# Kernel optimization log

Measured on AMD Instinct MI355X. Metric: run time of the kernel, lower is better.

Reference implementation:

```python
import jax, jax.numpy as jnp
import numpy as np


def setup_inputs() -> dict:
    key = jax.random.key(0)
    ks = jax.random.split(key, 6)
    B, N_IN, N_OUT, C_IN, C_OUT, S, NNZ = 16, 6250, 25000, 64, 64, 9, 75000
    x = jax.random.normal(ks[0], (B, N_IN, C_IN), dtype=jnp.float32)
    trans_values = jax.random.uniform(ks[1], (NNZ,), dtype=jnp.float32)
    trans_row = jax.random.randint(ks[2], (NNZ,), 0, N_OUT, dtype=jnp.int32)
    trans_col = jax.random.randint(ks[3], (NNZ,), 0, N_IN, dtype=jnp.int32)
    spiral_indices = jax.random.randint(ks[4], (N_OUT, S), 0, N_OUT, dtype=jnp.int32)
    # Linear(S*C_IN -> C_OUT), kaiming-ish scale
    W = jax.random.normal(ks[5], (S * C_IN, C_OUT), dtype=jnp.float32) * (1.0 / np.sqrt(S * C_IN))
    b = jnp.zeros((C_OUT,), dtype=jnp.float32)
    return {"x": x, "trans_values": trans_values, "trans_row": trans_row,
            "trans_col": trans_col, "spiral_indices": spiral_indices,
            "W": W, "b": b, "n_out": N_OUT}


def reference(x, trans_values, trans_row, trans_col, spiral_indices, W, b, n_out):
    B, N_in, C = x.shape
    # Pool: gather cols, scale by sparse values, scatter-add to rows
    gathered = x[:, trans_col, :] * trans_values[None, :, None]        # [B, nnz, C]
    pooled = jnp.zeros((B, n_out, C), x.dtype).at[:, trans_row].add(gathered)  # [B, n_out, C]
    # SpiralConv: gather spiral neighborhoods, flatten, linear
    S = spiral_indices.shape[1]
    feat = pooled[:, spiral_indices, :].reshape(B, n_out, S * C)       # [B, n_out, S*C]
    out = feat @ W + b                                                 # [B, n_out, C_out]
    return jax.nn.elu(out)
```

## Files before the change

### kernel.cpp

```cpp
#include <hip/hip_runtime.h>

#define B_     16
#define N_IN_  6250
#define N_OUT_ 25000
#define C_     64
#define S_     9
#define NNZ_   75000
#define MT_    391
#define BROW_  584

typedef __bf16 bf16x8 __attribute__((ext_vector_type(8)));
typedef float floatx4 __attribute__((ext_vector_type(4)));

__device__ inline void async_copy16(const void* g, void* l) {
    __builtin_amdgcn_global_load_lds(
        (const __attribute__((address_space(1))) void*)g,
        (__attribute__((address_space(3))) void*)l, 16, 0, 0);
}


__global__ void hist_kernel(const int* __restrict__ rows, int* __restrict__ counts, int nnz) {
    int i = blockIdx.x * blockDim.x + threadIdx.x;
    if (i < nnz) atomicAdd(&counts[rows[i]], 1);
}

__global__ void scan1_kernel(const int* __restrict__ counts, int* __restrict__ offsets,
                             int* __restrict__ bsum, int n) {
    __shared__ int wsum[16];
    int t = threadIdx.x;
    int wid = t >> 6, lane = t & 63;
    int i = blockIdx.x * 1024 + t;
    int v = (i < n) ? counts[i] : 0;
    int s = v;
    #pragma unroll
    for (int d = 1; d < 64; d <<= 1) {
        int u = __shfl_up(s, d, 64);
        if (lane >= d) s += u;
    }
    if (lane == 63) wsum[wid] = s;
    __syncthreads();
    if (wid == 0 && lane < 16) {
        int ws = wsum[lane];
        #pragma unroll
        for (int d = 1; d < 16; d <<= 1) {
            int u = __shfl_up(ws, d, 64);
            if (lane >= d) ws += u;
        }
        wsum[lane] = ws;
    }
    __syncthreads();
    int wave_off = (wid == 0) ? 0 : wsum[wid - 1];
    int incl = s + wave_off;
    if (i < n) offsets[i] = incl - v;
    if (t == 1023) bsum[blockIdx.x] = incl;
}

__global__ void scan2_kernel(int* __restrict__ bsum, int* __restrict__ offsets, int nblk, int n) {
    if (threadIdx.x == 0) {
        int t = 0;
        for (int i = 0; i < nblk; ++i) { int v = bsum[i]; bsum[i] = t; t += v; }
        offsets[n] = t;
    }
}

__global__ void scan3_kernel(int* __restrict__ offsets, const int* __restrict__ bsum,
                             int* __restrict__ cursor, int n) {
    int i = blockIdx.x * 1024 + threadIdx.x;
    if (i < n) {
        int o = offsets[i] + bsum[blockIdx.x];
        offsets[i] = o;
        cursor[i] = o;
    }
}

__global__ void fill_kernel(const int* __restrict__ rows, const int* __restrict__ cols,
                            const float* __restrict__ vals, int* __restrict__ cursor,
                            int* __restrict__ ecol, float* __restrict__ eval, int nnz) {
    int i = blockIdx.x * blockDim.x + threadIdx.x;
    if (i < nnz) {
        int p = atomicAdd(&cursor[rows[i]], 1);
        ecol[p] = cols[i];
        eval[p] = vals[i];
    }
}

__global__ __launch_bounds__(256) void pool_kernel(
        const float* __restrict__ x, const int* __restrict__ offsets,
        const int* __restrict__ ecol, const float* __restrict__ eval,
        __bf16* __restrict__ pooled) {
    __shared__ int   scol[64];
    __shared__ float sval[64];
    int row = blockIdx.x;
    int t = threadIdx.x;
    int c = t & 63, bq = t >> 6;
    int beg = offsets[row], end = offsets[row + 1];
    int count = end - beg;

    float acc[4] = {0.f, 0.f, 0.f, 0.f};
    for (int base = 0; base < count; base += 64) {
        int nb = min(64, count - base);
        if (t < nb) {
            scol[t] = ecol[beg + base + t];
            sval[t] = eval[beg + base + t];
        }
        __syncthreads();
        for (int k = 0; k < nb; ++k) {
            int col = scol[k];
            float v = sval[k];
            const float* xp = x + ((size_t)col * C_ + c);
            #pragma unroll
            for (int j = 0; j < 4; ++j) {
                acc[j] += xp[(size_t)(bq * 4 + j) * N_IN_ * C_] * v;
            }
        }
        __syncthreads();
    }
    #pragma unroll
    for (int j = 0; j < 4; ++j) {
        pooled[((size_t)(bq * 4 + j) * N_OUT_ + row) * C_ + c] = (__bf16)acc[j];
    }
}

__global__ void convw_kernel(const float* __restrict__ W, __bf16* __restrict__ Wt) {
    int i = blockIdx.x * blockDim.x + threadIdx.x;
    if (i < 576 * 64) {
        int k = i >> 6, n = i & 63;
        Wt[n * 576 + k] = (__bf16)W[i];
    }
}

__global__ __launch_bounds__(256, 2) void gemm_kernel(
        const __bf16* __restrict__ pooled, const int* __restrict__ spiral,
        const __bf16* __restrict__ Wt, const float* __restrict__ bias,
        float* __restrict__ out) {
    __shared__ __bf16 Bs[64 * BROW_];

    int bx = blockIdx.x;
    int xcd = bx & 7;
    int rr = bx >> 3;
    int half = (rr >= MT_) ? 1 : 0;
    int mt = rr - half * MT_;
    int b = xcd + 8 * half;

    int t = threadIdx.x;
    int wave = t >> 6, lane = t & 63;
    int quad = lane >> 4, l16 = lane & 15;
    int mbase = mt * 64 + wave * 16;
    int m = mbase + l16;
    int mc = (m < N_OUT_) ? m : 0;

    for (int j = t; j < (64 * BROW_ * 2) / 16; j += 256) {
        int col = j / 73;
        int rem = j - col * 73;
        async_copy16((const char*)Wt + col * 1152 + rem * 16,
                     (char*)Bs + j * 16);
    }

    int src[S_];
    #pragma unroll
    for (int s = 0; s < S_; ++s) src[s] = spiral[mc * S_ + s];

    const __bf16* poolb = pooled + (size_t)b * N_OUT_ * C_;

    __syncthreads();

    floatx4 acc[4] = {};
    bf16x8 Acur[2], Anxt[2];

    auto loadA = [&](int s, bf16x8* A) {
        const __bf16* p = poolb + (size_t)src[s] * C_ + quad * 8;
        A[0] = *reinterpret_cast<const bf16x8*>(p);
        A[1] = *reinterpret_cast<const bf16x8*>(p + 32);
    };

    loadA(0, Acur);
    #pragma unroll
    for (int s = 0; s < S_; ++s) {
        if (s + 1 < S_) {
            loadA(s + 1, (s & 1) ? Acur : Anxt);
            __builtin_amdgcn_sched_barrier(0);
        }
        bf16x8* A = (s & 1) ? Anxt : Acur;
        #pragma unroll
        for (int kc = 0; kc < 2; ++kc) {
            #pragma unroll
            for (int nt = 0; nt < 4; ++nt) {
                bf16x8 bb = *reinterpret_cast<const bf16x8*>(
                    &Bs[(nt * 16 + l16) * BROW_ + s * 64 + kc * 32 + quad * 8]);
                acc[nt] = __builtin_amdgcn_mfma_f32_16x16x32_bf16(A[kc], bb, acc[nt], 0, 0, 0);
            }
        }
    }

    float* outb = out + (size_t)b * N_OUT_ * C_;
    #pragma unroll
    for (int nt = 0; nt < 4; ++nt) {
        float bn = bias[nt * 16 + l16];
        #pragma unroll
        for (int i = 0; i < 4; ++i) {
            int mm = mbase + quad * 4 + i;
            if (mm < N_OUT_) {
                float v = acc[nt][i] + bn;
                v = (v > 0.0f) ? v : expm1f(v);
                outb[(size_t)mm * C_ + nt * 16 + l16] = v;
            }
        }
    }
}

extern "C" void kernel_launch(void* const* d_in, const int* in_sizes, int n_in,
                              void* d_out, int out_size, void* d_ws, size_t ws_size,
                              hipStream_t stream) {
    const float* x      = (const float*)d_in[0];
    const float* tvals  = (const float*)d_in[1];
    const int*   trow   = (const int*)d_in[2];
    const int*   tcol   = (const int*)d_in[3];
    const int*   spiral = (const int*)d_in[4];
    const float* W      = (const float*)d_in[5];
    const float* bias   = (const float*)d_in[6];
    float* out = (float*)d_out;

    char* ws = (char*)d_ws;
    size_t off = 0;
    auto alloc = [&](size_t bytes) -> void* {
        void* p = ws + off;
        off += (bytes + 255) & ~(size_t)255;
        return p;
    };
    __bf16* pooled  = (__bf16*)alloc((size_t)B_ * N_OUT_ * C_ * 2);
    __bf16* Wt      = (__bf16*)alloc(576 * 64 * 2);
    int*    cursor  = (int*)alloc(N_OUT_ * 4);
    int*    offsets = (int*)alloc((N_OUT_ + 1) * 4);
    int*    ecol    = (int*)alloc(NNZ_ * 4);
    float*  eval    = (float*)alloc(NNZ_ * 4);
    int*    counts  = (int*)alloc(N_OUT_ * 4);
    int*    bsum    = (int*)alloc(32 * 4);

    const int NBLK = (N_OUT_ + 1023) / 1024;
    hipMemsetAsync(counts, 0, N_OUT_ * 4, stream);
    hist_kernel<<<(NNZ_ + 255) / 256, 256, 0, stream>>>(trow, counts, NNZ_);
    scan1_kernel<<<NBLK, 1024, 0, stream>>>(counts, offsets, bsum, N_OUT_);
    scan2_kernel<<<1, 64, 0, stream>>>(bsum, offsets, NBLK, N_OUT_);
    scan3_kernel<<<NBLK, 1024, 0, stream>>>(offsets, bsum, cursor, N_OUT_);
    fill_kernel<<<(NNZ_ + 255) / 256, 256, 0, stream>>>(trow, tcol, tvals, cursor, ecol, eval, NNZ_);
    pool_kernel<<<N_OUT_, 256, 0, stream>>>(x, offsets, ecol, eval, pooled);
    convw_kernel<<<(576 * 64 + 255) / 256, 256, 0, stream>>>(W, Wt);
    gemm_kernel<<<8 * (2 * MT_), 256, 0, stream>>>(pooled, spiral, Wt, bias, out);
}
```

Before: 300.5 us.

## Widen GEMM tile to 256 rows per block and vectorize pooling per wave

The GEMM block now computes 256 output rows (four 16-row sub-tiles per wave), so each B fragment read from LDS feeds four MFMAs. The weights are pre-packed into a fragment-friendly layout and loaded with a contiguous async copy. Pooling now gives one wave to each output row, with each lane owning one batch and 16 channels, using float4 loads and bf16x8 stores in place of scalar loads and shared staging. The trade-offs are higher register pressure and fewer blocks, plus vector spiral-index loads that assume int4 alignment on a 36-byte stride.

```diff
diff --git a/kernel.cpp b/kernel.cpp
--- a/kernel.cpp
+++ b/kernel.cpp
@@ -6,8 +6,7 @@
 #define C_     64
 #define S_     9
 #define NNZ_   75000
-#define MT_    391
-#define BROW_  584
+#define MT2_   98
 
 typedef __bf16 bf16x8 __attribute__((ext_vector_type(8)));
 typedef float floatx4 __attribute__((ext_vector_type(4)));
@@ -88,89 +87,100 @@
         const float* __restrict__ x, const int* __restrict__ offsets,
         const int* __restrict__ ecol, const float* __restrict__ eval,
         __bf16* __restrict__ pooled) {
-    __shared__ int   scol[64];
-    __shared__ float sval[64];
-    int row = blockIdx.x;
     int t = threadIdx.x;
-    int c = t & 63, bq = t >> 6;
+    int wid = t >> 6, lane = t & 63;
+    int row = blockIdx.x * 4 + wid;
+    int b = lane >> 2;
+    int cq = (lane & 3) << 4;
     int beg = offsets[row], end = offsets[row + 1];
-    int count = end - beg;
-
-    float acc[4] = {0.f, 0.f, 0.f, 0.f};
-    for (int base = 0; base < count; base += 64) {
-        int nb = min(64, count - base);
-        if (t < nb) {
-            scol[t] = ecol[beg + base + t];
-            sval[t] = eval[beg + base + t];
-        }
-        __syncthreads();
-        for (int k = 0; k < nb; ++k) {
-            int col = scol[k];
-            float v = sval[k];
-            const float* xp = x + ((size_t)col * C_ + c);
-            #pragma unroll
-            for (int j = 0; j < 4; ++j) {
-                acc[j] += xp[(size_t)(bq * 4 + j) * N_IN_ * C_] * v;
-            }
-        }
-        __syncthreads();
-    }
+
+    const float* xb = x + (size_t)b * N_IN_ * C_ + cq;
+    floatx4 acc[4] = {};
+
+    int col = 0; float v = 0.f;
+    if (beg < end) { col = ecol[beg]; v = eval[beg]; }
+    for (int k = beg; k < end; ++k) {
+        int col2 = 0; float v2 = 0.f;
+        if (k + 1 < end) { col2 = ecol[k + 1]; v2 = eval[k + 1]; }
+        const floatx4* xp = reinterpret_cast<const floatx4*>(xb + (size_t)col * C_);
+        #pragma unroll
+        for (int j = 0; j < 4; ++j) acc[j] += xp[j] * v;
+        col = col2; v = v2;
+    }
+
+    __bf16* op = pooled + ((size_t)b * N_OUT_ + row) * C_ + cq;
+    bf16x8 o0, o1;
     #pragma unroll
     for (int j = 0; j < 4; ++j) {
-        pooled[((size_t)(bq * 4 + j) * N_OUT_ + row) * C_ + c] = (__bf16)acc[j];
-    }
-}
-
-__global__ void convw_kernel(const float* __restrict__ W, __bf16* __restrict__ Wt) {
+        o0[j]     = (__bf16)acc[0][j];
+        o0[j + 4] = (__bf16)acc[1][j];
+        o1[j]     = (__bf16)acc[2][j];
+        o1[j + 4] = (__bf16)acc[3][j];
+    }
+    *reinterpret_cast<bf16x8*>(op)     = o0;
+    *reinterpret_cast<bf16x8*>(op + 8) = o1;
+}
+
+__global__ void convw_kernel(const float* __restrict__ W, __bf16* __restrict__ WtF) {
     int i = blockIdx.x * blockDim.x + threadIdx.x;
-    if (i < 576 * 64) {
-        int k = i >> 6, n = i & 63;
-        Wt[n * 576 + k] = (__bf16)W[i];
+    if (i < 72 * 64 * 8) {
+        int kb = i >> 9;
+        int n  = (i >> 3) & 63;
+        int j  = i & 7;
+        WtF[i] = (__bf16)W[(kb * 8 + j) * 64 + n];
     }
 }
 
 __global__ __launch_bounds__(256, 2) void gemm_kernel(
         const __bf16* __restrict__ pooled, const int* __restrict__ spiral,
-        const __bf16* __restrict__ Wt, const float* __restrict__ bias,
+        const __bf16* __restrict__ WtF, const float* __restrict__ bias,
         float* __restrict__ out) {
-    __shared__ __bf16 Bs[64 * BROW_];
+    __shared__ __bf16 Bs[72 * 64 * 8];
 
     int bx = blockIdx.x;
     int xcd = bx & 7;
     int rr = bx >> 3;
-    int half = (rr >= MT_) ? 1 : 0;
-    int mt = rr - half * MT_;
+    int half = (rr >= MT2_) ? 1 : 0;
+    int mt = rr - half * MT2_;
     int b = xcd + 8 * half;
 
     int t = threadIdx.x;
     int wave = t >> 6, lane = t & 63;
     int quad = lane >> 4, l16 = lane & 15;
-    int mbase = mt * 64 + wave * 16;
-    int m = mbase + l16;
-    int mc = (m < N_OUT_) ? m : 0;
-
-    for (int j = t; j < (64 * BROW_ * 2) / 16; j += 256) {
-        int col = j / 73;
-        int rem = j - col * 73;
-        async_copy16((const char*)Wt + col * 1152 + rem * 16,
-                     (char*)Bs + j * 16);
-    }
-
-    int src[S_];
-    #pragma unroll
-    for (int s = 0; s < S_; ++s) src[s] = spiral[mc * S_ + s];
-
+    int mbase = mt * 256 + wave * 64;
+
+    #pragma unroll
+    for (int j = 0; j < 18; ++j) {
+        int idx = t + j * 256;
+        async_copy16((const char*)WtF + (size_t)idx * 16, (char*)Bs + idx * 16);
+    }
+
+    int src[4][S_];
+    #pragma unroll
+    for (int mi = 0; mi < 4; ++mi) {
+        int m = mbase + mi * 16 + l16;
+        int mc = (m < N_OUT_) ? m : 0;
+        const int* sp = spiral + (size_t)mc * S_;
+        int4 a0 = *reinterpret_cast<const int4*>(sp);
+        int4 a1 = *reinterpret_cast<const int4*>(sp + 4);
+        src[mi][0] = a0.x; src[mi][1] = a0.y; src[mi][2] = a0.z; src[mi][3] = a0.w;
+        src[mi][4] = a1.x; src[mi][5] = a1.y; src[mi][6] = a1.z; src[mi][7] = a1.w;
+        src[mi][8] = sp[8];
+    }
     const __bf16* poolb = pooled + (size_t)b * N_OUT_ * C_;
 
     __syncthreads();
 
-    floatx4 acc[4] = {};
-    bf16x8 Acur[2], Anxt[2];
-
-    auto loadA = [&](int s, bf16x8* A) {
-        const __bf16* p = poolb + (size_t)src[s] * C_ + quad * 8;
-        A[0] = *reinterpret_cast<const bf16x8*>(p);
-        A[1] = *reinterpret_cast<const bf16x8*>(p + 32);
+    floatx4 acc[4][4] = {};
+    bf16x8 Acur[4][2], Anxt[4][2];
+
+    auto loadA = [&](int s, bf16x8 (*A)[2]) {
+        #pragma unroll
+        for (int mi = 0; mi < 4; ++mi) {
+            const __bf16* p = poolb + (size_t)src[mi][s] * C_ + quad * 8;
+            A[mi][0] = *reinterpret_cast<const bf16x8*>(p);
+            A[mi][1] = *reinterpret_cast<const bf16x8*>(p + 32);
+        }
     };
 
     loadA(0, Acur);
@@ -180,29 +190,36 @@
             loadA(s + 1, (s & 1) ? Acur : Anxt);
             __builtin_amdgcn_sched_barrier(0);
         }
-        bf16x8* A = (s & 1) ? Anxt : Acur;
+        bf16x8 (*A)[2] = (s & 1) ? Anxt : Acur;
         #pragma unroll
         for (int kc = 0; kc < 2; ++kc) {
             #pragma unroll
             for (int nt = 0; nt < 4; ++nt) {
+                int kb = s * 8 + kc * 4 + quad;
                 bf16x8 bb = *reinterpret_cast<const bf16x8*>(
-                    &Bs[(nt * 16 + l16) * BROW_ + s * 64 + kc * 32 + quad * 8]);
-                acc[nt] = __builtin_amdgcn_mfma_f32_16x16x32_bf16(A[kc], bb, acc[nt], 0, 0, 0);
+                    Bs + (((kb << 6) + (nt << 4) + l16) << 3));
+                #pragma unroll
+                for (int mi = 0; mi < 4; ++mi)
+                    acc[mi][nt] = __builtin_amdgcn_mfma_f32_16x16x32_bf16(
+                        A[mi][kc], bb, acc[mi][nt], 0, 0, 0);
             }
         }
     }
 
     float* outb = out + (size_t)b * N_OUT_ * C_;
     #pragma unroll
-    for (int nt = 0; nt < 4; ++nt) {
-        float bn = bias[nt * 16 + l16];
-        #pragma unroll
-        for (int i = 0; i < 4; ++i) {
-            int mm = mbase + quad * 4 + i;
-            if (mm < N_OUT_) {
-                float v = acc[nt][i] + bn;
-                v = (v > 0.0f) ? v : expm1f(v);
-                outb[(size_t)mm * C_ + nt * 16 + l16] = v;
+    for (int mi = 0; mi < 4; ++mi) {
+        #pragma unroll
+        for (int nt = 0; nt < 4; ++nt) {
+            float bn = bias[nt * 16 + l16];
+            #pragma unroll
+            for (int i = 0; i < 4; ++i) {
+                int mm = mbase + mi * 16 + quad * 4 + i;
+                if (mm < N_OUT_) {
+                    float v = acc[mi][nt][i] + bn;
+                    v = (v > 0.0f) ? v : expm1f(v);
+                    outb[(size_t)mm * C_ + nt * 16 + l16] = v;
+                }
             }
         }
     }
@@ -228,7 +245,7 @@
         return p;
     };
     __bf16* pooled  = (__bf16*)alloc((size_t)B_ * N_OUT_ * C_ * 2);
-    __bf16* Wt      = (__bf16*)alloc(576 * 64 * 2);
+    __bf16* WtF     = (__bf16*)alloc(72 * 64 * 8 * 2);
     int*    cursor  = (int*)alloc(N_OUT_ * 4);
     int*    offsets = (int*)alloc((N_OUT_ + 1) * 4);
     int*    ecol    = (int*)alloc(NNZ_ * 4);
@@ -243,7 +260,7 @@
     scan2_kernel<<<1, 64, 0, stream>>>(bsum, offsets, NBLK, N_OUT_);
     scan3_kernel<<<NBLK, 1024, 0, stream>>>(offsets, bsum, cursor, N_OUT_);
     fill_kernel<<<(NNZ_ + 255) / 256, 256, 0, stream>>>(trow, tcol, tvals, cursor, ecol, eval, NNZ_);
-    pool_kernel<<<N_OUT_, 256, 0, stream>>>(x, offsets, ecol, eval, pooled);
-    convw_kernel<<<(576 * 64 + 255) / 256, 256, 0, stream>>>(W, Wt);
-    gemm_kernel<<<8 * (2 * MT_), 256, 0, stream>>>(pooled, spiral, Wt, bias, out);
-}
+    pool_kernel<<<N_OUT_ / 4, 256, 0, stream>>>(x, offsets, ecol, eval, pooled);
+    convw_kernel<<<(72 * 64 * 8 + 255) / 256, 256, 0, stream>>>(W, WtF);
+    gemm_kernel<<<8 * (2 * MT2_), 256, 0, stream>>>(pooled, spiral, WtF, bias, out);
+}
```

Result: faster. 288.3 us (-4.1%).
